# Optimization experiments

Measured on AMD Instinct MI355X. Metric: run time of the kernel, lower is better.

Reference implementation:

```python
import jax, jax.numpy as jnp
import numpy as np

K = 3; PAD = 1; STRIDE = 1; EPS = 1e-5


def setup_inputs() -> dict:
    key = jax.random.key(0)
    k0, k1, k2 = jax.random.split(key, 3)
    B, C, H, W, O = 4, 256, 64, 64, 256
    x = jax.random.normal(k0, (B, C, H, W), jnp.float32)
    # offset conv: small random weights so offsets are nontrivial but bounded
    w_off = jax.random.normal(k1, (2 * K * K, C, K, K), jnp.float32) * 0.01
    b_off = jnp.zeros((2 * K * K,), jnp.float32)
    # kaiming normal, mode=fan_out: std = sqrt(2 / (O*K*K))
    w_def = jax.random.normal(k2, (O, C, K, K), jnp.float32) * np.float32(np.sqrt(2.0 / (O * K * K)))
    gamma = jnp.ones((O,), jnp.float32)
    beta = jnp.zeros((O,), jnp.float32)
    return {"x": x, "w_off": w_off, "b_off": b_off, "w_def": w_def, "gamma": gamma, "beta": beta}


def _bilinear_gather(x, py, px):
    """x: [B,C,H,W]; py,px: [B,K2,Ho,Wo] float sample coords.
    Returns [B,K2,Ho,Wo,C] with zero padding outside (per-corner masking,
    matching torchvision deform_conv2d)."""
    B, C, H, W = x.shape
    y0f = jnp.floor(py); x0f = jnp.floor(px)
    wy1 = py - y0f; wy0 = 1.0 - wy1
    wx1 = px - x0f; wx0 = 1.0 - wx1
    bidx = jnp.arange(B)[:, None, None, None]

    def corner(yf, xf, wgt):
        valid = (yf >= 0) & (yf <= H - 1) & (xf >= 0) & (xf <= W - 1)
        yc = jnp.clip(yf.astype(jnp.int32), 0, H - 1)
        xc = jnp.clip(xf.astype(jnp.int32), 0, W - 1)
        v = x[bidx, :, yc, xc]  # [B,K2,Ho,Wo,C] (advanced idx moves C last)
        return v * (wgt * valid)[..., None]

    return (corner(y0f, x0f, wy0 * wx0) + corner(y0f, x0f + 1.0, wy0 * wx1)
            + corner(y0f + 1.0, x0f, wy1 * wx0) + corner(y0f + 1.0, x0f + 1.0, wy1 * wx1))


def _forward(x, w_off, b_off, w_def, gamma, beta):
    B, C, H, W = x.shape
    O = w_def.shape[0]
    K2 = K * K
    # 1) offset-predicting conv
    off = jax.lax.conv_general_dilated(x, w_off, (STRIDE, STRIDE), ((PAD, PAD), (PAD, PAD)))
    off = off + b_off[None, :, None, None]
    Ho, Wo = off.shape[2], off.shape[3]
    off = off.reshape(B, K2, 2, Ho, Wo)  # pairs (dy, dx) per kernel tap
    # 2) deformable sampling locations
    ky, kx = jnp.meshgrid(jnp.arange(K, dtype=jnp.float32), jnp.arange(K, dtype=jnp.float32), indexing='ij')
    base_y = (jnp.arange(Ho, dtype=jnp.float32) * STRIDE - PAD)
    base_x = (jnp.arange(Wo, dtype=jnp.float32) * STRIDE - PAD)
    py = off[:, :, 0] + ky.reshape(K2)[None, :, None, None] + base_y[None, None, :, None]
    px = off[:, :, 1] + kx.reshape(K2)[None, :, None, None] + base_x[None, None, None, :]
    vals = _bilinear_gather(x, py, px)  # [B,K2,Ho,Wo,C]
    # 3) deform conv GEMM (bias=False)
    out = jnp.einsum('bkhwc,ock->bohw', vals, w_def.reshape(O, C, K2))
    # 4) BatchNorm (training mode: batch stats) + ReLU
    mean = out.mean(axis=(0, 2, 3))
    var = out.var(axis=(0, 2, 3))
    out = (out - mean[None, :, None, None]) * (gamma * jax.lax.rsqrt(var + EPS))[None, :, None, None]
    out = out + beta[None, :, None, None]
    return jax.nn.relu(out)


def reference(x, w_off, b_off, w_def, gamma, beta):
    return _forward(x, w_off, b_off, w_def, gamma, beta)
```

## Files before the change

### kernel.cpp

```cpp
#include <hip/hip_runtime.h>
#include <hip/hip_bf16.h>

typedef unsigned int  uint;
typedef unsigned short ushort;
typedef short bf16x8 __attribute__((ext_vector_type(8)));
typedef float f32x4  __attribute__((ext_vector_type(4)));

#define HW   4096
#define KD   2304

__device__ __forceinline__ void load_lds16(const void* g, void* l) {
    __builtin_amdgcn_global_load_lds((const __attribute__((address_space(1))) void*)g,
                                     (__attribute__((address_space(3))) void*)l, 16, 0, 0);
}
__device__ __forceinline__ float blo(uint u) { return __uint_as_float(u << 16); }
__device__ __forceinline__ float bhi(uint u) { return __uint_as_float(u & 0xffff0000u); }
__device__ __forceinline__ uint pack2(float e, float o) {
    __hip_bfloat16 he = __float2bfloat16(e), ho = __float2bfloat16(o);
    return (uint)(*(ushort*)&he) | ((uint)(*(ushort*)&ho) << 16);
}

__global__ void prep_x2t(const float* __restrict__ x, uint* __restrict__ x2t) {
    __shared__ uint tl[32][65];
    int bidx = blockIdx.x;
    int ab  = bidx & 63;
    int cpb = (bidx >> 6) & 3;
    int b   = bidx >> 8;
    int t = threadIdx.x;
#pragma unroll
    for (int i = 0; i < 8; ++i) {
        int idx = i * 256 + t;
        int cp = idx >> 6, a = idx & 63;
        const float* p = x + ((size_t)(b * 256 + (cpb * 32 + cp) * 2)) * HW + ab * 64 + a;
        tl[cp][a] = pack2(p[0], p[HW]);
    }
    __syncthreads();
#pragma unroll
    for (int i = 0; i < 8; ++i) {
        int idx = i * 256 + t;
        int a = idx >> 5, cp = idx & 31;
        x2t[((size_t)b * 4096 + ab * 64 + a) * 128 + cpb * 32 + cp] = tl[cp][a];
    }
}

__global__ void prep_bt(const float* __restrict__ w_def, ushort* __restrict__ bt) {
    int idx = blockIdx.x * 256 + threadIdx.x;
    int c   = idx & 255;
    int tap = (idx >> 8) % 9;
    int o   = idx / KD;
    __hip_bfloat16 h = __float2bfloat16(w_def[(o * 256 + c) * 9 + tap]);
    bt[idx] = *(ushort*)&h;
}

__global__ void prep_bt0(const float* __restrict__ w_off, ushort* __restrict__ bt0) {
    int idx = blockIdx.x * 256 + threadIdx.x;
    int c   = idx & 255;
    int tap = (idx >> 8) % 9;
    int j   = idx / KD;
    float v = (j < 18) ? w_off[(j * 256 + c) * 9 + tap] : 0.f;
    __hip_bfloat16 h = __float2bfloat16(v);
    bt0[idx] = *(ushort*)&h;
}

__global__ __launch_bounds__(512) void gemm_off(const uint* __restrict__ x2t,
                                                const ushort* __restrict__ bt0,
                                                const float* __restrict__ b_off,
                                                float* __restrict__ off) {
    int id = blockIdx.x;
    int xcd = id & 7;
    int b = xcd >> 1, h = (xcd & 1) * 32 + (id >> 3);
    int t = threadIdx.x, wv = t >> 6, lane = t & 63;
    int mrow = lane & 15, quad = lane >> 4;
    int mq = wv & 3, nn = wv >> 2;

    __shared__ uint   lX[3 * 64 * 32];
    __shared__ ushort lB[32 * 576];

    f32x4 acc = {0.f, 0.f, 0.f, 0.f};

    for (int cb = 0; cb < 4; ++cb) {
#pragma unroll
        for (int s = 0; s < 3; ++s) {
            int q   = s * 8 + wv;
            int dy  = q >> 3;
            int y   = h + dy - 1;
            int sub = q & 7;
            int wl  = sub * 8 + (lane >> 3);
            int cps = ((lane & 7) ^ ((lane >> 3) & 7)) * 4;
            if ((unsigned)y < 64u) {
                const uint* src = x2t + ((size_t)(b * 4096 + y * 64 + wl)) * 128 + cb * 32 + cps;
                load_lds16(src, &lX[q * 256]);
            } else {
                uint4 z = {0u, 0u, 0u, 0u};
                *(uint4*)&lX[q * 256 + lane * 4] = z;
            }
        }
#pragma unroll
        for (int s = 0; s < 5; ++s) {
            int q = s * 8 + wv;
            if (q < 36) {
                int e = q * 512 + lane * 8;
                int o  = e / 576;
                int r  = e - o * 576;
                int chp = r >> 3;
                int ch  = chp ^ (o & 7);
                int tap = ch >> 3, k8 = ch & 7;
                const ushort* src = bt0 + (size_t)o * KD + tap * 256 + cb * 64 + k8 * 8;
                load_lds16(src, &lB[q * 512]);
            }
        }
        __syncthreads();

#pragma unroll
        for (int tap = 0; tap < 9; ++tap) {
            int dy = tap / 3, dx = tap % 3;
            int xx = mq * 16 + mrow + dx - 1;
            bool vx = (unsigned)xx < 64u;
            int xc = min(max(xx, 0), 63);
#pragma unroll
            for (int kb = 0; kb < 2; ++kb) {
                int cp0 = kb * 16 + quad * 4;
                uint4 ad = {0u, 0u, 0u, 0u};
                if (vx) ad = *(const uint4*)&lX[dy * 2048 + xc * 32 + (cp0 ^ ((xc & 7) * 4))];
                bf16x8 af = *(bf16x8*)&ad;
                int o = nn * 16 + mrow;
                int chs = (tap * 8 + (((kb * 4 + quad)) ^ (o & 7)));
                bf16x8 bfr = *(const bf16x8*)&lB[o * 576 + chs * 8];
                acc = __builtin_amdgcn_mfma_f32_16x16x32_bf16(af, bfr, acc, 0, 0, 0);
            }
        }
        __syncthreads();
    }
    {
        int o = nn * 16 + mrow;
        float bias = (o < 18) ? b_off[o] : 0.f;
        f32x4 v = acc;
        v.x += bias; v.y += bias; v.z += bias; v.w += bias;
        int wpos = mq * 16 + quad * 4;
        *(f32x4*)(off + ((size_t)(b * 32 + o)) * HW + h * 64 + wpos) = v;
    }
}

__global__ __launch_bounds__(1024, 4) void fused_main(const uint* __restrict__ x2t,
                                                      const ushort* __restrict__ bt,
                                                      const float* __restrict__ off,
                                                      float* __restrict__ out,
                                                      float* __restrict__ stats) {
    int id = blockIdx.x;
    int xcd = id & 7;
    int b = xcd >> 1, h = (xcd & 1) * 32 + (id >> 3);
    int t = threadIdx.x;
    int wv = t >> 6, lane = t & 63;
    int mrow = lane & 15, quad = lane >> 4;
    bool producer = (wv < 8);
    int ppos = (wv << 3) + (lane >> 3);
    int pc8  = lane & 7;

    __shared__ int    sAc[4][9][64];
    __shared__ float  sWc[4][9][64];
    __shared__ ushort lA[2][64 * 64];
    __shared__ ushort lB[2][256 * 64];

    for (int i = t; i < 576; i += 1024) {
        int tap = i >> 6, ww = i & 63;
        int hw = h * 64 + ww;
        float oy = off[((size_t)(b * 32 + 2 * tap)) * HW + hw];
        float ox = off[((size_t)(b * 32 + 2 * tap + 1)) * HW + hw];
        float py = oy + (float)(tap / 3 + h - 1);
        float px = ox + (float)(tap % 3 + ww - 1);
        float y0f = floorf(py), x0f = floorf(px);
        float wy1 = py - y0f, wx1 = px - x0f;
        float wy0 = 1.f - wy1, wx0 = 1.f - wx1;
        bool vy0 = (y0f >= 0.f) && (y0f <= 63.f);
        bool vy1 = (y0f >= -1.f) && (y0f <= 62.f);
        bool vx0 = (x0f >= 0.f) && (x0f <= 63.f);
        bool vx1 = (x0f >= -1.f) && (x0f <= 62.f);
        int iy0 = min(max((int)y0f, 0), 63),  iy1 = min(max((int)y0f + 1, 0), 63);
        int ix0 = min(max((int)x0f, 0), 63),  ix1 = min(max((int)x0f + 1, 0), 63);
        sAc[0][tap][ww] = iy0 * 64 + ix0;
        sAc[1][tap][ww] = iy0 * 64 + ix1;
        sAc[2][tap][ww] = iy1 * 64 + ix0;
        sAc[3][tap][ww] = iy1 * 64 + ix1;
        sWc[0][tap][ww] = wy0 * wx0 * (float)(vy0 && vx0);
        sWc[1][tap][ww] = wy0 * wx1 * (float)(vy0 && vx1);
        sWc[2][tap][ww] = wy1 * wx0 * (float)(vy1 && vx0);
        sWc[3][tap][ww] = wy1 * wx1 * (float)(vy1 && vx1);
    }
    __syncthreads();

    f32x4 acc[4][2];
#pragma unroll
    for (int m = 0; m < 4; ++m)
#pragma unroll
        for (int n = 0; n < 2; ++n) acc[m][n] = {0.f, 0.f, 0.f, 0.f};

    const uint* xb = x2t + (size_t)b * 4096 * 128;

    auto issue_gathers = [&](int sl, uint4 (&g)[4]) {
        int tap = sl >> 2, cb = sl & 3;
        const uint* xp = xb + cb * 32 + pc8 * 4;
        g[0] = *(const uint4*)(xp + (size_t)sAc[0][tap][ppos] * 128);
        g[1] = *(const uint4*)(xp + (size_t)sAc[1][tap][ppos] * 128);
        g[2] = *(const uint4*)(xp + (size_t)sAc[2][tap][ppos] * 128);
        g[3] = *(const uint4*)(xp + (size_t)sAc[3][tap][ppos] * 128);
    };
    auto issue_B = [&](int sl, ushort* lBb) {
        int tap = sl >> 2, cb = sl & 3;
#pragma unroll
        for (int s2 = 0; s2 < 4; ++s2) {
            int e = s2 * 512 + t;
            int o = e >> 3, pp = e & 7;
            int k8 = pp ^ (o & 7);
            const ushort* src = bt + (size_t)o * KD + tap * 256 + cb * 64 + k8 * 8;
            load_lds16(src, &lBb[(e & ~63) * 8]);
        }
    };
    auto finish = [&](int sl, ushort* lAb, const uint4 (&g)[4]) {
        int tap = sl >> 2;
        float f0 = sWc[0][tap][ppos], f1 = sWc[1][tap][ppos];
        float f2 = sWc[2][tap][ppos], f3 = sWc[3][tap][ppos];
        const uint* c0 = (const uint*)&g[0];
        const uint* c1 = (const uint*)&g[1];
        const uint* c2 = (const uint*)&g[2];
        const uint* c3 = (const uint*)&g[3];
        uint r[4];
#pragma unroll
        for (int j = 0; j < 4; ++j) {
            float ev = f0 * blo(c0[j]) + f1 * blo(c1[j]) + f2 * blo(c2[j]) + f3 * blo(c3[j]);
            float ov = f0 * bhi(c0[j]) + f1 * bhi(c1[j]) + f2 * bhi(c2[j]) + f3 * bhi(c3[j]);
            r[j] = pack2(ev, ov);
        }
        uint4 gg = {r[0], r[1], r[2], r[3]};
        *(uint4*)&lAb[ppos * 64 + ((pc8 ^ (ppos & 7)) * 8)] = gg;
    };
    auto mfma_pass = [&](int bi) {
        int wvc = wv - 8;
#pragma unroll
        for (int kb = 0; kb < 2; ++kb) {
            bf16x8 af[4];
#pragma unroll
            for (int m = 0; m < 4; ++m) {
                int r = m * 16 + mrow;
                af[m] = *(const bf16x8*)&lA[bi][r * 64 + (((kb * 4 + quad) ^ (r & 7)) * 8)];
            }
#pragma unroll
            for (int n = 0; n < 2; ++n) {
                int r = wvc * 32 + n * 16 + mrow;
                bf16x8 bfr = *(const bf16x8*)&lB[bi][r * 64 + (((kb * 4 + quad) ^ (r & 7)) * 8)];
#pragma unroll
                for (int m = 0; m < 4; ++m)
                    acc[m][n] = __builtin_amdgcn_mfma_f32_16x16x32_bf16(af[m], bfr, acc[m][n], 0, 0, 0);
            }
        }
    };

    uint4 gA[4], gB[4];
    if (producer) {
        issue_gathers(0, gA);
        issue_B(0, lB[0]);
        finish(0, lA[0], gA);
        issue_gathers(1, gB);
    }

    for (int s = 0; s < 36; s += 2) {
        __syncthreads();
        if (producer) {
            issue_B(s + 1, lB[1]);
            if (s + 2 < 36) issue_gathers(s + 2, gA);
            finish(s + 1, lA[1], gB);
        } else {
            mfma_pass(0);
        }
        __syncthreads();
        if (producer) {
            if (s + 2 < 36) {
                issue_B(s + 2, lB[0]);
                if (s + 3 < 36) issue_gathers(s + 3, gB);
                finish(s + 2, lA[0], gA);
            }
        } else {
            mfma_pass(1);
        }
    }

    if (!producer) {
        int wvc = wv - 8;
#pragma unroll
        for (int n = 0; n < 2; ++n) {
            int o = wvc * 32 + n * 16 + mrow;
            float ss = 0.f, qq = 0.f;
#pragma unroll
            for (int m = 0; m < 4; ++m) {
                int pos = m * 16 + quad * 4;
                f32x4 v = acc[m][n];
                *(f32x4*)(out + ((size_t)(b * 256 + o)) * HW + h * 64 + pos) = v;
                ss += v.x + v.y + v.z + v.w;
                qq += v.x * v.x + v.y * v.y + v.z * v.z + v.w * v.w;
            }
            ss += __shfl_xor(ss, 16); ss += __shfl_xor(ss, 32);
            qq += __shfl_xor(qq, 16); qq += __shfl_xor(qq, 32);
            if (quad == 0) {
                atomicAdd(&stats[o], ss);
                atomicAdd(&stats[512 + o], qq);
            }
        }
    }
}

__global__ void bn_finalize(const float* __restrict__ stats,
                            const float* __restrict__ gamma,
                            float* __restrict__ ms) {
    int o = threadIdx.x;
    float S = stats[o], S2 = stats[512 + o];
    float m  = S / 16384.f;
    float var = S2 / 16384.f - m * m;
    ms[o]       = m;
    ms[256 + o] = gamma[o] * rsqrtf(var + 1e-5f);
}

__global__ void bn_apply(float* __restrict__ out,
                         const float* __restrict__ ms,
                         const float* __restrict__ beta) {
    int idx4 = blockIdx.x * 256 + threadIdx.x;
    int o = (idx4 >> 10) & 255;
    float4 v = ((const float4*)out)[idx4];
    float mu = ms[o], sc = ms[256 + o], be = beta[o];
    v.x = fmaxf((v.x - mu) * sc + be, 0.f);
    v.y = fmaxf((v.y - mu) * sc + be, 0.f);
    v.z = fmaxf((v.z - mu) * sc + be, 0.f);
    v.w = fmaxf((v.w - mu) * sc + be, 0.f);
    ((float4*)out)[idx4] = v;
}

extern "C" void kernel_launch(void* const* d_in, const int* in_sizes, int n_in,
                              void* d_out, int out_size, void* d_ws, size_t ws_size,
                              hipStream_t stream) {
    const float* x     = (const float*)d_in[0];
    const float* w_off = (const float*)d_in[1];
    const float* b_off = (const float*)d_in[2];
    const float* w_def = (const float*)d_in[3];
    const float* gamma = (const float*)d_in[4];
    const float* beta  = (const float*)d_in[5];
    float* out = (float*)d_out;

    char* ws = (char*)d_ws;
    uint*   x2t   = (uint*)ws;
    ushort* bt    = (ushort*)(ws + 8388608);
    ushort* bt0   = (ushort*)(ws + 9568256);
    float*  off   = (float*)(ws + 9715712);
    float*  stats = (float*)(ws + 11812864);
    float*  ms    = (float*)(ws + 11816960);

    hipMemsetAsync(stats, 0, 4096, stream);
    prep_x2t<<<1024, 256, 0, stream>>>(x, x2t);
    prep_bt <<<2304, 256, 0, stream>>>(w_def, bt);
    prep_bt0<<<288,  256, 0, stream>>>(w_off, bt0);
    gemm_off<<<256, 512, 0, stream>>>(x2t, bt0, b_off, off);
    fused_main<<<256, 1024, 0, stream>>>(x2t, bt, off, out, stats);
    bn_finalize<<<1, 256, 0, stream>>>(stats, gamma, ms);
    bn_apply<<<4096, 256, 0, stream>>>(out, ms, beta);
}
```

Before: 168.4 us.

## Load weight fragments directly into consumer registers instead of staging through LDS

Removes the LDS double-buffer for the weight (B) tile, which the producer waves used to fill through global_load_lds. Each consumer wave now loads its own B fragments straight from global memory into registers one stage ahead, then feeds them to the MFMAs. This frees LDS, lowers block LDS usage and removes producer issue work and LDS read traffic. In exchange it adds per-wave uncoalesced global loads (16-byte chunks strided by KD) and more consumer VGPRs, and a load may not finish before the MFMAs that need it.

Measured after the change: 212.6 us. +26.2%, slower.

```diff
diff --git a/kernel.cpp b/kernel.cpp
--- a/kernel.cpp
+++ b/kernel.cpp
@@ -155,11 +155,11 @@
     bool producer = (wv < 8);
     int ppos = (wv << 3) + (lane >> 3);
     int pc8  = lane & 7;
+    int wvc  = wv - 8;
 
     __shared__ int    sAc[4][9][64];
     __shared__ float  sWc[4][9][64];
     __shared__ ushort lA[2][64 * 64];
-    __shared__ ushort lB[2][256 * 64];
 
     for (int i = t; i < 576; i += 1024) {
         int tap = i >> 6, ww = i & 63;
@@ -204,17 +204,6 @@
         g[2] = *(const uint4*)(xp + (size_t)sAc[2][tap][ppos] * 128);
         g[3] = *(const uint4*)(xp + (size_t)sAc[3][tap][ppos] * 128);
     };
-    auto issue_B = [&](int sl, ushort* lBb) {
-        int tap = sl >> 2, cb = sl & 3;
-#pragma unroll
-        for (int s2 = 0; s2 < 4; ++s2) {
-            int e = s2 * 512 + t;
-            int o = e >> 3, pp = e & 7;
-            int k8 = pp ^ (o & 7);
-            const ushort* src = bt + (size_t)o * KD + tap * 256 + cb * 64 + k8 * 8;
-            load_lds16(src, &lBb[(e & ~63) * 8]);
-        }
-    };
     auto finish = [&](int sl, ushort* lAb, const uint4 (&g)[4]) {
         int tap = sl >> 2;
         float f0 = sWc[0][tap][ppos], f1 = sWc[1][tap][ppos];
@@ -233,8 +222,18 @@
         uint4 gg = {r[0], r[1], r[2], r[3]};
         *(uint4*)&lAb[ppos * 64 + ((pc8 ^ (ppos & 7)) * 8)] = gg;
     };
-    auto mfma_pass = [&](int bi) {
-        int wvc = wv - 8;
+    auto loadB = [&](int sl, bf16x8 (&br)[4]) {
+        int tap = sl >> 2, cb = sl & 3;
+        const ushort* base = bt + tap * 256 + cb * 64 + quad * 8;
+#pragma unroll
+        for (int kb = 0; kb < 2; ++kb)
+#pragma unroll
+            for (int n = 0; n < 2; ++n) {
+                int r = wvc * 32 + n * 16 + mrow;
+                br[kb * 2 + n] = *(const bf16x8*)(base + (size_t)r * KD + kb * 32);
+            }
+    };
+    auto mfma_pass = [&](int bi, const bf16x8 (&br)[4]) {
 #pragma unroll
         for (int kb = 0; kb < 2; ++kb) {
             bf16x8 af[4];
@@ -244,47 +243,43 @@
                 af[m] = *(const bf16x8*)&lA[bi][r * 64 + (((kb * 4 + quad) ^ (r & 7)) * 8)];
             }
 #pragma unroll
-            for (int n = 0; n < 2; ++n) {
-                int r = wvc * 32 + n * 16 + mrow;
-                bf16x8 bfr = *(const bf16x8*)&lB[bi][r * 64 + (((kb * 4 + quad) ^ (r & 7)) * 8)];
+            for (int n = 0; n < 2; ++n)
 #pragma unroll
                 for (int m = 0; m < 4; ++m)
-                    acc[m][n] = __builtin_amdgcn_mfma_f32_16x16x32_bf16(af[m], bfr, acc[m][n], 0, 0, 0);
-            }
+                    acc[m][n] = __builtin_amdgcn_mfma_f32_16x16x32_bf16(af[m], br[kb * 2 + n], acc[m][n], 0, 0, 0);
         }
     };
 
     uint4 gA[4], gB[4];
+    bf16x8 brA[4], brB[4];
     if (producer) {
         issue_gathers(0, gA);
-        issue_B(0, lB[0]);
         finish(0, lA[0], gA);
         issue_gathers(1, gB);
+    } else {
+        loadB(0, brA);
     }
 
     for (int s = 0; s < 36; s += 2) {
         __syncthreads();
         if (producer) {
-            issue_B(s + 1, lB[1]);
             if (s + 2 < 36) issue_gathers(s + 2, gA);
             finish(s + 1, lA[1], gB);
         } else {
-            mfma_pass(0);
+            loadB(s + 1, brB);
+            mfma_pass(0, brA);
         }
         __syncthreads();
         if (producer) {
-            if (s + 2 < 36) {
-                issue_B(s + 2, lB[0]);
-                if (s + 3 < 36) issue_gathers(s + 3, gB);
-                finish(s + 2, lA[0], gA);
-            }
+            if (s + 3 < 36) issue_gathers(s + 3, gB);
+            if (s + 2 < 36) finish(s + 2, lA[0], gA);
         } else {
-            mfma_pass(1);
+            if (s + 2 < 36) loadB(s + 2, brA);
+            mfma_pass(1, brB);
         }
     }
 
     if (!producer) {
-        int wvc = wv - 8;
 #pragma unroll
         for (int n = 0; n < 2; ++n) {
             int o = wvc * 32 + n * 16 + mrow;
```
